# Optimization experiments

Hardware: AMD Instinct MI355X
Metric: run time of the kernel (lower is better)

The kernel has to match this reference:

```python
import jax, jax.numpy as jnp
import numpy as np

# _norm_l1l2l3(l1=1, l2=1, l3=2) = 3/4 (computed from the factorial/double-factorial formula)
NORM = 0.75

N, IN1, IN2, KOUT = 512, 128, 128, 128


def setup_inputs() -> dict:
    key = jax.random.key(0)
    k1, k2, k3 = jax.random.split(key, 3)
    x = jax.random.normal(k1, (N, 3, IN1), dtype=jnp.float32)
    y = jax.random.normal(k2, (N, 3, IN2), dtype=jnp.float32)
    w = jax.random.normal(k3, (IN1, IN2, KOUT), dtype=jnp.float32)
    a = jnp.float32(1.0)
    return {"w": w, "a": a, "x": x, "y": y}


def reference(w, a, x, y):
    # contraction1: outer product over the two Cartesian axes (l1=1, l2=1 -> l3=2)
    # x: [n, i=3, a], y: [n, j=3, b] -> out1: [n, 3, 3, a, b]
    out1 = jnp.einsum("nia,njb->nijab", x, y)
    # contraction2: weighted contraction of feature channels with scaled weights
    # (w*a): [a, b, k], out1: [n, 3, 3, a, b] -> [n, 3, 3, k]
    out2 = NORM * jnp.einsum("abk,nijab->nijk", w * a, out1)
    return (out1, out2)
```

## Files before the change

### kernel.cpp

```cpp
#include <hip/hip_runtime.h>
#include <stdint.h>

typedef __attribute__((ext_vector_type(8))) short bf16x8;
typedef __attribute__((ext_vector_type(4))) float f32x4;

static constexpr int O1_ELEMS    = 512*3*3*128*128;
static constexpr int WB2_FLOATS  = 1048576;
static constexpr int P_FLOATS    = 512*9*128;
static constexpr int NSEG        = 8;
static constexpr size_t SCRATCH_BYTES = (size_t)WB2_FLOATS*4 + (size_t)NSEG*P_FLOATS*4;
static constexpr int NTILES      = 4608;
static constexpr int SKIP_TILES  = 352;
static constexpr int S1 = 1152, S2 = 1728;
static constexpr int NCOMP       = 384;

__device__ inline unsigned short f32_to_bf16(float f) {
    union { float f; uint32_t u; } v; v.f = f;
    uint32_t r = v.u + 0x7FFF + ((v.u >> 16) & 1);
    return (unsigned short)(r >> 16);
}

__device__ inline bf16x8 bf16x8_from_f32(const float* p) {
    float4 v0 = *(const float4*)p;
    float4 v1 = *(const float4*)(p + 4);
    union { bf16x8 v; unsigned short s[8]; } u;
    u.s[0] = f32_to_bf16(v0.x); u.s[1] = f32_to_bf16(v0.y);
    u.s[2] = f32_to_bf16(v0.z); u.s[3] = f32_to_bf16(v0.w);
    u.s[4] = f32_to_bf16(v1.x); u.s[5] = f32_to_bf16(v1.y);
    u.s[6] = f32_to_bf16(v1.z); u.s[7] = f32_to_bf16(v1.w);
    return u.v;
}

__device__ inline void write_tile(int tile, const float* __restrict__ x,
                                  const float* __restrict__ y,
                                  float* __restrict__ out1, int t) {
    const f32x4* y4 = (const f32x4*)y;
    f32x4* o4 = (f32x4*)out1;
    const int b4 = t & 31, a0 = t >> 5;
    int n  = tile / 9;
    int ij = tile - n * 9;
    int i  = ij / 3, j = ij - i * 3;
    f32x4 yv = y4[(n * 3 + j) * 32 + b4];
    const float* xrow = x + (n * 3 + i) * 128;
    f32x4* dst = o4 + (size_t)tile * 4096 + a0 * 32 + b4;
    #pragma unroll
    for (int p = 0; p < 16; ++p) {
        float xs = xrow[p * 8 + a0];
        f32x4 r = yv * xs;
        __builtin_nontemporal_store(r, dst);
        dst += 256;
    }
}

__device__ inline void conv_block(int a, int t, const float* __restrict__ w,
                                  unsigned short* __restrict__ wb2) {
    __shared__ unsigned short lt[128][132];
    const float4* src = (const float4*)(w + (size_t)a * 16384);
    #pragma unroll
    for (int it = 0; it < 16; ++it) {
        int fidx = it * 256 + t;
        float4 v = src[fidx];
        int b = fidx >> 5, k4 = fidx & 31;
        unsigned short* d = &lt[b][k4 * 4];
        d[0] = f32_to_bf16(v.x); d[1] = f32_to_bf16(v.y);
        d[2] = f32_to_bf16(v.z); d[3] = f32_to_bf16(v.w);
    }
    __syncthreads();
    const int k = t >> 1, bh = t & 1;
    uint4* dst = (uint4*)(wb2 + (size_t)a * 16384 + (size_t)k * 128 + bh * 64);
    #pragma unroll
    for (int i8 = 0; i8 < 8; ++i8) {
        uint32_t pk[4];
        #pragma unroll
        for (int q = 0; q < 4; ++q) {
            uint32_t lo = lt[bh * 64 + i8 * 8 + q * 2][k];
            uint32_t hi = lt[bh * 64 + i8 * 8 + q * 2 + 1][k];
            pk[q] = lo | (hi << 16);
        }
        uint4 vv = {pk[0], pk[1], pk[2], pk[3]};
        dst[i8] = vv;
    }
}

__device__ inline void comp_block(int bid, int tid, const float* __restrict__ x,
                                  const float* __restrict__ y,
                                  const unsigned short* __restrict__ wb2,
                                  float* __restrict__ partial) {
    __shared__ float xshc[16][3][64];
    const int aseg = bid & 7;
    const int kt   = (bid >> 3) & 1;
    const int mt   = bid >> 4;
    const int l    = tid & 63;
    const int wv   = tid >> 6;
    const int l15  = l & 15, lg = l >> 4;

    bf16x8 afrag[4][4];
    #pragma unroll
    for (int Mt = 0; Mt < 4; ++Mt)
        #pragma unroll
        for (int ks = 0; ks < 4; ++ks)
            afrag[Mt][ks] = bf16x8_from_f32(
                y + (size_t)(mt * 64 + Mt * 16 + l15) * 128 + ks * 32 + lg * 8);

    #pragma unroll
    for (int p = 0; p < 12; ++p) {
        int e = tid + p * 256;
        int ac = e / 192, r = e - ac * 192, i = r >> 6, mm = r & 63;
        int n = (mt * 64 + mm) / 3;
        xshc[ac][i][mm] = x[n * 384 + i * 128 + aseg * 16 + ac];
    }
    __syncthreads();

    float acc2[3][4][4] = {};
    const unsigned short* wbase =
        wb2 + (size_t)(kt * 64 + wv * 16 + l15) * 128 + lg * 8;

    #pragma unroll 2
    for (int ac = 0; ac < 16; ++ac) {
        const int a = aseg * 16 + ac;
        const unsigned short* wp = wbase + (size_t)a * 16384;
        bf16x8 bf0 = *(const bf16x8*)(wp);
        bf16x8 bf1 = *(const bf16x8*)(wp + 32);
        bf16x8 bf2 = *(const bf16x8*)(wp + 64);
        bf16x8 bf3 = *(const bf16x8*)(wp + 96);

        f32x4 tt[4] = {{0.f,0.f,0.f,0.f},{0.f,0.f,0.f,0.f},
                       {0.f,0.f,0.f,0.f},{0.f,0.f,0.f,0.f}};
        #pragma unroll
        for (int Mt = 0; Mt < 4; ++Mt) {
            tt[Mt] = __builtin_amdgcn_mfma_f32_16x16x32_bf16(afrag[Mt][0], bf0, tt[Mt], 0, 0, 0);
            tt[Mt] = __builtin_amdgcn_mfma_f32_16x16x32_bf16(afrag[Mt][1], bf1, tt[Mt], 0, 0, 0);
            tt[Mt] = __builtin_amdgcn_mfma_f32_16x16x32_bf16(afrag[Mt][2], bf2, tt[Mt], 0, 0, 0);
            tt[Mt] = __builtin_amdgcn_mfma_f32_16x16x32_bf16(afrag[Mt][3], bf3, tt[Mt], 0, 0, 0);
        }

        #pragma unroll
        for (int i = 0; i < 3; ++i)
            #pragma unroll
            for (int Mt = 0; Mt < 4; ++Mt) {
                float4 xv = *(const float4*)&xshc[ac][i][Mt * 16 + lg * 4];
                acc2[i][Mt][0] += xv.x * tt[Mt][0];
                acc2[i][Mt][1] += xv.y * tt[Mt][1];
                acc2[i][Mt][2] += xv.z * tt[Mt][2];
                acc2[i][Mt][3] += xv.w * tt[Mt][3];
            }
    }

    float* pp = partial + (size_t)aseg * P_FLOATS;
    const int kcol = kt * 64 + wv * 16 + l15;
    #pragma unroll
    for (int i = 0; i < 3; ++i)
        #pragma unroll
        for (int Mt = 0; Mt < 4; ++Mt)
            #pragma unroll
            for (int r = 0; r < 4; ++r) {
                int m = mt * 64 + Mt * 16 + lg * 4 + r;
                int n = m / 3, j = m - 3 * n;
                pp[((size_t)(n * 3 + i) * 3 + j) * 128 + kcol] = acc2[i][Mt][r];
            }
}

__global__ __launch_bounds__(256) void k1_kernel(const float* __restrict__ w,
                                                 const float* __restrict__ x,
                                                 const float* __restrict__ y,
                                                 unsigned short* __restrict__ wb2,
                                                 float* __restrict__ out1, int t0) {
    const int b = (int)blockIdx.x;
    if (b < 128) { conv_block(b, (int)threadIdx.x, w, wb2); return; }
    write_tile(t0 + b - 128, x, y, out1, (int)threadIdx.x);
}

__global__ __launch_bounds__(256) void k2_kernel(const float* __restrict__ x,
                                                 const float* __restrict__ y,
                                                 const unsigned short* __restrict__ wb2,
                                                 float* __restrict__ partial,
                                                 float* __restrict__ out1, int t0) {
    const int b = (int)blockIdx.x;
    if (b < NCOMP) { comp_block(b, (int)threadIdx.x, x, y, wb2, partial); return; }
    write_tile(t0 + b - NCOMP, x, y, out1, (int)threadIdx.x);
}

__global__ __launch_bounds__(256) void k3_kernel(const float* __restrict__ a_s,
                                                 const float* __restrict__ partial,
                                                 const float* __restrict__ x,
                                                 const float* __restrict__ y,
                                                 float* __restrict__ out1,
                                                 float* __restrict__ out2,
                                                 int t0, int ntiles) {
    const int b = (int)blockIdx.x;
    const int e = b * 256 + (int)threadIdx.x;
    float s = 0.f;
    #pragma unroll
    for (int sg = 0; sg < NSEG; ++sg) s += partial[(size_t)sg * P_FLOATS + e];
    out2[e] = 0.75f * a_s[0] * s;
    if (b < ntiles)
        write_tile(t0 + b, x, y, out1, (int)threadIdx.x);
}

__global__ __launch_bounds__(256) void finish_kernel(const float* __restrict__ x,
                                                     const float* __restrict__ y,
                                                     float* __restrict__ out1) {
    write_tile((int)blockIdx.x, x, y, out1, (int)threadIdx.x);
}

extern "C" void kernel_launch(void* const* d_in, const int* in_sizes, int n_in,
                              void* d_out, int out_size, void* d_ws, size_t ws_size,
                              hipStream_t stream) {
    const float* w  = (const float*)d_in[0];
    const float* as = (const float*)d_in[1];
    const float* x  = (const float*)d_in[2];
    const float* y  = (const float*)d_in[3];
    float* out1 = (float*)d_out;
    float* out2 = out1 + O1_ELEMS;

    const bool have_ws = (ws_size >= SCRATCH_BYTES);
    unsigned short* wb2;
    float* partial;
    int t0;
    if (have_ws) {
        wb2 = (unsigned short*)d_ws;
        partial = (float*)d_ws + WB2_FLOATS;
        t0 = 0;
    } else {
        wb2 = (unsigned short*)out1;
        partial = out1 + WB2_FLOATS;
        t0 = SKIP_TILES;
    }
    const int s3 = NTILES - t0 - S1 - S2;

    k1_kernel<<<128 + S1, 256, 0, stream>>>(w, x, y, wb2, out1, t0);
    k2_kernel<<<NCOMP + S2, 256, 0, stream>>>(x, y, wb2, partial, out1, t0 + S1);
    k3_kernel<<<2304, 256, 0, stream>>>(as, partial, x, y, out1, out2, t0 + S1 + S2, s3);
    if (!have_ws)
        finish_kernel<<<SKIP_TILES, 256, 0, stream>>>(x, y, out1);
}
```

Before: 72.54 us.

## Replace partial-sum buffer and reduce kernel with atomic accumulation into out2

```diff
diff --git a/kernel.cpp b/kernel.cpp
--- a/kernel.cpp
+++ b/kernel.cpp
@@ -7,12 +7,11 @@
 static constexpr int O1_ELEMS    = 512*3*3*128*128;
 static constexpr int WB2_FLOATS  = 1048576;
 static constexpr int P_FLOATS    = 512*9*128;
-static constexpr int NSEG        = 8;
-static constexpr size_t SCRATCH_BYTES = (size_t)WB2_FLOATS*4 + (size_t)NSEG*P_FLOATS*4;
+static constexpr size_t SCRATCH_BYTES = (size_t)WB2_FLOATS*4;
 static constexpr int NTILES      = 4608;
-static constexpr int SKIP_TILES  = 352;
-static constexpr int S1 = 1152, S2 = 1728;
-static constexpr int NCOMP       = 384;
+static constexpr int SKIP_TILES  = 64;
+static constexpr int S1          = 1200;
+static constexpr int NZB         = 36;
 
 __device__ inline unsigned short f32_to_bf16(float f) {
     union { float f; uint32_t u; } v; v.f = f;
@@ -52,9 +51,9 @@
     }
 }
 
-__device__ inline void conv_block(int a, int t, const float* __restrict__ w,
-                                  unsigned short* __restrict__ wb2) {
-    __shared__ unsigned short lt[128][132];
+__device__ inline void conv_role(int a, int t, const float* __restrict__ w,
+                                 unsigned short* __restrict__ wb2, char* smem) {
+    unsigned short (*lt)[132] = (unsigned short (*)[132])smem;
     const float4* src = (const float4*)(w + (size_t)a * 16384);
     #pragma unroll
     for (int it = 0; it < 16; ++it) {
@@ -82,14 +81,15 @@
     }
 }
 
-__device__ inline void comp_block(int bid, int tid, const float* __restrict__ x,
-                                  const float* __restrict__ y,
-                                  const unsigned short* __restrict__ wb2,
-                                  float* __restrict__ partial) {
-    __shared__ float xshc[16][3][64];
-    const int aseg = bid & 7;
-    const int kt   = (bid >> 3) & 1;
-    const int mt   = bid >> 4;
+__device__ inline void comp_role(int cb, int tid, float alpha,
+                                 const float* __restrict__ x,
+                                 const float* __restrict__ y,
+                                 const unsigned short* __restrict__ wb2,
+                                 float* __restrict__ out2, char* smem) {
+    float (*xshc)[3][64] = (float (*)[3][64])smem;
+    const int aseg = cb & 7;
+    const int kt   = (cb >> 3) & 1;
+    const int mt   = cb >> 4;
     const int l    = tid & 63;
     const int wv   = tid >> 6;
     const int l15  = l & 15, lg = l >> 4;
@@ -146,7 +146,6 @@
             }
     }
 
-    float* pp = partial + (size_t)aseg * P_FLOATS;
     const int kcol = kt * 64 + wv * 16 + l15;
     #pragma unroll
     for (int i = 0; i < 3; ++i)
@@ -156,7 +155,8 @@
             for (int r = 0; r < 4; ++r) {
                 int m = mt * 64 + Mt * 16 + lg * 4 + r;
                 int n = m / 3, j = m - 3 * n;
-                pp[((size_t)(n * 3 + i) * 3 + j) * 128 + kcol] = acc2[i][Mt][r];
+                unsafeAtomicAdd(&out2[((size_t)(n * 3 + i) * 3 + j) * 128 + kcol],
+                                alpha * acc2[i][Mt][r]);
             }
 }
 
@@ -164,37 +164,38 @@
                                                  const float* __restrict__ x,
                                                  const float* __restrict__ y,
                                                  unsigned short* __restrict__ wb2,
-                                                 float* __restrict__ out1, int t0) {
+                                                 float* __restrict__ out1,
+                                                 float* __restrict__ out2, int t0) {
+    __shared__ __align__(16) char smem[33792];
     const int b = (int)blockIdx.x;
-    if (b < 128) { conv_block(b, (int)threadIdx.x, w, wb2); return; }
-    write_tile(t0 + b - 128, x, y, out1, (int)threadIdx.x);
-}
-
-__global__ __launch_bounds__(256) void k2_kernel(const float* __restrict__ x,
+    const int t = (int)threadIdx.x;
+    if (b < 128) { conv_role(b, t, w, wb2, smem); return; }
+    if (b < 128 + NZB) {
+        f32x4* o2 = (f32x4*)out2;
+        const f32x4 z = {0.f, 0.f, 0.f, 0.f};
+        #pragma unroll
+        for (int p = 0; p < 16; ++p)
+            o2[(size_t)(b - 128) * 4096 + p * 256 + t] = z;
+        return;
+    }
+    write_tile(t0 + b - 128 - NZB, x, y, out1, t);
+}
+
+__global__ __launch_bounds__(256) void k2_kernel(const float* __restrict__ a_s,
+                                                 const float* __restrict__ x,
                                                  const float* __restrict__ y,
                                                  const unsigned short* __restrict__ wb2,
-                                                 float* __restrict__ partial,
-                                                 float* __restrict__ out1, int t0) {
+                                                 float* __restrict__ out1,
+                                                 float* __restrict__ out2, int t0) {
+    __shared__ __align__(16) char smem[12288];
     const int b = (int)blockIdx.x;
-    if (b < NCOMP) { comp_block(b, (int)threadIdx.x, x, y, wb2, partial); return; }
-    write_tile(t0 + b - NCOMP, x, y, out1, (int)threadIdx.x);
-}
-
-__global__ __launch_bounds__(256) void k3_kernel(const float* __restrict__ a_s,
-                                                 const float* __restrict__ partial,
-                                                 const float* __restrict__ x,
-                                                 const float* __restrict__ y,
-                                                 float* __restrict__ out1,
-                                                 float* __restrict__ out2,
-                                                 int t0, int ntiles) {
-    const int b = (int)blockIdx.x;
-    const int e = b * 256 + (int)threadIdx.x;
-    float s = 0.f;
-    #pragma unroll
-    for (int sg = 0; sg < NSEG; ++sg) s += partial[(size_t)sg * P_FLOATS + e];
-    out2[e] = 0.75f * a_s[0] * s;
-    if (b < ntiles)
-        write_tile(t0 + b, x, y, out1, (int)threadIdx.x);
+    const int t = (int)threadIdx.x;
+    if (b < 384) {
+        const float alpha = 0.75f * a_s[0];
+        comp_role(b, t, alpha, x, y, wb2, out2, smem);
+        return;
+    }
+    write_tile(t0 + S1 + (b - 384), x, y, out1, t);
 }
 
 __global__ __launch_bounds__(256) void finish_kernel(const float* __restrict__ x,
@@ -214,23 +215,12 @@
     float* out2 = out1 + O1_ELEMS;
 
     const bool have_ws = (ws_size >= SCRATCH_BYTES);
-    unsigned short* wb2;
-    float* partial;
-    int t0;
-    if (have_ws) {
-        wb2 = (unsigned short*)d_ws;
-        partial = (float*)d_ws + WB2_FLOATS;
-        t0 = 0;
-    } else {
-        wb2 = (unsigned short*)out1;
-        partial = out1 + WB2_FLOATS;
-        t0 = SKIP_TILES;
-    }
-    const int s3 = NTILES - t0 - S1 - S2;
-
-    k1_kernel<<<128 + S1, 256, 0, stream>>>(w, x, y, wb2, out1, t0);
-    k2_kernel<<<NCOMP + S2, 256, 0, stream>>>(x, y, wb2, partial, out1, t0 + S1);
-    k3_kernel<<<2304, 256, 0, stream>>>(as, partial, x, y, out1, out2, t0 + S1 + S2, s3);
+    unsigned short* wb2 = have_ws ? (unsigned short*)d_ws : (unsigned short*)out1;
+    const int t0 = have_ws ? 0 : SKIP_TILES;
+    const int s2 = NTILES - t0 - S1;
+
+    k1_kernel<<<128 + NZB + S1, 256, 0, stream>>>(w, x, y, wb2, out1, out2, t0);
+    k2_kernel<<<384 + s2, 256, 0, stream>>>(as, x, y, wb2, out1, out2, t0);
     if (!have_ws)
         finish_kernel<<<SKIP_TILES, 256, 0, stream>>>(x, y, out1);
 }
```

New measurement: 77.58 us. +7.0%, slower.
